# Kernel tuning notes

Measured on AMD Instinct MI355X. Metric: run time of the kernel, lower is better.

Reference implementation:

```python
import jax, jax.numpy as jnp
import numpy as np

THRESH = 0.5
POOL_K = 8  # feature_hw // proto_grid = 128 // 16
EPS = 1e-4
NEG = -1e30


def _avg_pool(x, k):
    # x: [n, c, h, w] -> [n, c, h//k, w//k]
    n, c, h, w = x.shape
    return x.reshape(n, c, h // k, k, w // k, k).mean(axis=(3, 5))


def reference(qry, sup_x, sup_y):
    # squeeze as in forward
    qry = qry[:, 0]          # [B=1, C, H, W]
    sup_x = sup_x[0, :, 0]   # [shot, C, H, W]
    sup_y = sup_y[0]         # [shot, 1, H, W]

    shot, nch, H, W = sup_x.shape

    # grid prototypes via avg pooling
    n_sup = _avg_pool(sup_x, POOL_K)                      # [shot, C, gh, gw]
    y_g = _avg_pool(sup_y, POOL_K)                        # [shot, 1, gh, gw]

    cand = n_sup.reshape(shot, nch, -1).transpose(0, 2, 1).reshape(-1, nch)  # [M, C]
    y_flat = y_g.reshape(-1)                              # [M]

    # threshold mask with fallback chain (thresh -> 0.1 -> all), static shapes
    m1 = y_flat > THRESH
    m2 = y_flat > 0.1
    m_all = jnp.ones_like(m1)
    mask = jnp.where(jnp.any(m1), m1, jnp.where(jnp.any(m2), m2, m_all))  # [M]

    # mean-center and safe L2-normalize prototypes (per proto over channels)
    protos = cand - cand.mean(axis=-1, keepdims=True)
    pro_n = protos / jnp.maximum(jnp.linalg.norm(protos, axis=1, keepdims=True), EPS)  # [M, C]

    # mean-center and safe L2-normalize query (per pixel over channels)
    qc = qry - qry.mean(axis=1, keepdims=True)
    qry_n = qc / jnp.maximum(jnp.linalg.norm(qc, axis=1, keepdims=True), EPS)          # [B, C, H, W]

    # cosine-sim 1x1 conv = GEMM, scaled
    dists = jnp.einsum('bchw,mc->bmhw', qry_n, pro_n) * 20.0                           # [B, M, H, W]

    # masked softmax over prototypes (equivalent to selecting masked subset)
    logits = jnp.where(mask[None, :, None, None], dists, NEG)
    prob = jax.nn.softmax(logits, axis=1)                                              # [B, M, H, W]

    # weighted back-projection and final similarity map
    ch_proto = jnp.einsum('mc,bmhw->bchw', pro_n, prob)                                # [B, C, H, W]
    pred_grid = jnp.sum(qry_n * ch_proto * 20.0, axis=1, keepdims=True)                # [B, 1, H, W]
    return pred_grid


def setup_inputs() -> dict:
    key = jax.random.key(0)
    k1, k2, k3 = jax.random.split(key, 3)
    qry = jax.random.normal(k1, (1, 1, 256, 128, 128), dtype=jnp.float32)
    sup_x = jax.random.normal(k2, (1, 5, 1, 256, 128, 128), dtype=jnp.float32)
    sup_y = jax.random.uniform(k3, (1, 5, 1, 128, 128), dtype=jnp.float32)
    return {"qry": qry, "sup_x": sup_x, "sup_y": sup_y}
```

## Files before the change

kernel.cpp:

```cpp
#include <hip/hip_runtime.h>
#include <math.h>

typedef _Float16 f16x8 __attribute__((ext_vector_type(8)));
typedef float f32x4 __attribute__((ext_vector_type(4)));


__global__ __launch_bounds__(256) void pool_kernel(const float* __restrict__ sup_x,
                                                   const float* __restrict__ sup_y,
                                                   _Float16* __restrict__ pro_raw,
                                                   float* __restrict__ psum,
                                                   float* __restrict__ yv_ws) {
    const int b = blockIdx.x, t = threadIdx.x;
    if (b < 640) {
        __shared__ float hs[8192];
        __shared__ float xa[16][33];
        const int s = b >> 7, rem = b & 127;
        const int gy = rem >> 3, cq = rem & 7;
        const float* base = sup_x + ((size_t)(s * 256 + cq * 32) * 128 + gy * 8) * 128;
#pragma unroll 8
        for (int i = 0; i < 32; ++i) {
            const int run = i * 8 + (t >> 5);
            const float4 v = *(const float4*)(base + ((size_t)(run >> 3) * 128 + (run & 7)) * 128 + (t & 31) * 4);
            hs[i * 256 + t] = v.x + v.y + v.z + v.w;
        }
        __syncthreads();
#pragma unroll
        for (int e0 = 0; e0 < 2; ++e0) {
            const int e = e0 * 256 + t;
            const int c = e >> 4, gx = e & 15;
            float sum = 0.f;
#pragma unroll
            for (int r = 0; r < 8; ++r)
                sum += hs[(c * 8 + r) * 32 + gx * 2] + hs[(c * 8 + r) * 32 + gx * 2 + 1];
            xa[gx][c] = sum * (1.f / 64.f);
        }
        __syncthreads();
        const int mbase = s * 256 + gy * 16;
        if (t < 64) {
            const int gx = t >> 2, gi = t & 3;
            const int m = mbase + gx;
            const int g = cq * 4 + gi;
            f16x8 hv;
#pragma unroll
            for (int j = 0; j < 8; ++j) hv[j] = (_Float16)xa[gx][gi * 8 + j];
            *(f16x8*)(pro_raw + (size_t)m * 256 + (g << 3)) = hv;
        } else if (t < 80) {
            const int gx = t - 64;
            float s1 = 0.f, s2 = 0.f;
#pragma unroll
            for (int c = 0; c < 32; ++c) { const float x = xa[gx][c]; s1 += x; s2 += x * x; }
            const int m = mbase + gx;
            psum[m * 16 + cq * 2]     = s1;
            psum[m * 16 + cq * 2 + 1] = s2;
        }
    } else {
        const int r = b - 640;
        const int gy = t >> 4, gx = t & 15;
        const float* base = sup_y + r * 16384 + gy * 1024 + gx * 8;
        float sum = 0.f;
#pragma unroll
        for (int rr = 0; rr < 8; ++rr) {
            const float4 a = *(const float4*)(base + rr * 128);
            const float4 bb = *(const float4*)(base + rr * 128 + 4);
            sum += a.x + a.y + a.z + a.w + bb.x + bb.y + bb.z + bb.w;
        }
        yv_ws[r * 256 + t] = sum * (1.f / 64.f);
    }
}

__device__ __forceinline__ void gload_lds16h(const _Float16* g, _Float16* l) {
    __builtin_amdgcn_global_load_lds((const __attribute__((address_space(1))) unsigned int*)g,
                                     (__attribute__((address_space(3))) unsigned int*)l,
                                     16, 0, 0);
}
__device__ __forceinline__ void gload_lds16f(const float* g, float* l) {
    __builtin_amdgcn_global_load_lds((const __attribute__((address_space(1))) unsigned int*)g,
                                     (__attribute__((address_space(3))) unsigned int*)l,
                                     16, 0, 0);
}

__device__ __forceinline__ void stage_gather(const _Float16* __restrict__ pro_raw,
                                             const unsigned short* __restrict__ idxc,
                                             int tb, _Float16* dst, int w, int l) {
#pragma unroll
    for (int i = 0; i < 8; ++i) {
        const int off = w * 4096 + i * 512 + l * 8;
        const int rowp = off >> 8;
        const int m = idxc[tb + rowp];
        const int sc = (l & 31) ^ (rowp & 7);
        gload_lds16h(pro_raw + (size_t)m * 256 + (sc << 3), dst + off);
    }
}

__device__ __forceinline__ void compute_tile(const _Float16* __restrict__ pb,
                                             const float* __restrict__ alfc,
                                             int tilebase, int NA,
                                             const f16x8 (&bfr)[4][8],
                                             int row, int ln7, int lq, int w,
                                             float (&Sa)[4], float (&Wa)[4]) {
    f32x4 acc[4];
#pragma unroll
    for (int p = 0; p < 4; ++p) acc[p] = (f32x4){0.f, 0.f, 0.f, 0.f};
#pragma unroll
    for (int ks = 0; ks < 8; ++ks) {
        const int ch = (ks * 4 + lq) ^ ln7;
        const f16x8 a = *(const f16x8*)(pb + row * 256 + ch * 8);
#pragma unroll
        for (int p = 0; p < 4; ++p)
            acc[p] = __builtin_amdgcn_mfma_f32_16x16x32_f16(a, bfr[p][ks], acc[p], 0, 0, 0);
    }
    const int jb = tilebase + w * 16 + lq * 4;
    const f32x4 av = *(const f32x4*)(alfc + jb);
#pragma unroll
    for (int p = 0; p < 4; ++p) {
        float ssum = 0.f, wsum = 0.f;
#pragma unroll
        for (int r = 0; r < 4; ++r) {
            const float d = av[r] * acc[p][r];
            const float mk = (jb + r < NA) ? 1.f : 0.f;
            const float e = mk * __expf(d - 20.f);
            ssum += e; wsum += e * d;
        }
        Sa[p] += ssum; Wa[p] += wsum;
    }
}

__global__ __launch_bounds__(512, 2) void main_kernel(const float* __restrict__ qry,
                                                      const _Float16* __restrict__ pro_raw,
                                                      const float* __restrict__ psum,
                                                      const float* __restrict__ yv_ws,
                                                      float* __restrict__ out) {
    __shared__ __align__(16) _Float16 arena[65536];
    __shared__ __align__(16) float alfc[1408];
    __shared__ unsigned short idxc[1408];
    __shared__ int tot_s[20];
    __shared__ float scr[1024];
    __shared__ float2 stats[64];
    __shared__ int iflags[2];

    float*     qtf  = (float*)arena;
    _Float16*  qs   = arena + 32768;
    _Float16*  buf0 = arena;
    _Float16*  buf1 = arena + 32768;
    float*     red  = (float*)arena;

    const int t = threadIdx.x;
    const int w = t >> 6, l = t & 63;
    const int ln = l & 15, lq = l >> 4;
    const int ln7 = ln & 7;
    const int px0 = blockIdx.x * 64;

    if (t < 2) iflags[t] = 0;
    for (int i = t; i < 1408; i += 512) { alfc[i] = 0.f; idxc[i] = 0; }
    __syncthreads();

#pragma unroll
    for (int i = 0; i < 8; ++i) {
        const int c = i * 32 + (t >> 4);
        gload_lds16f(qry + (size_t)c * 16384 + px0 + (t & 15) * 4,
                     qtf + i * 2048 + t * 4);
    }

    float alf3[3], yv3[3];
    int f0 = 0, f1 = 0;
#pragma unroll
    for (int k = 0; k < 3; ++k) {
        const int m = t + k * 512;
        if (m < 1280) {
            float S1 = 0.f, S2 = 0.f;
            const f32x4* pp = (const f32x4*)(psum + m * 16);
#pragma unroll
            for (int u = 0; u < 4; ++u) {
                const f32x4 p = pp[u];
                S1 += p[0] + p[2]; S2 += p[1] + p[3];
            }
            alf3[k] = 20.f / fmaxf(sqrtf(fmaxf(S2 - S1 * S1 * (1.f / 256.f), 0.f)), 1e-4f);
            const float y = yv_ws[m];
            yv3[k] = y;
            if (y > 0.5f) f0 = 1;
            if (y > 0.1f) f1 = 1;
        }
    }
    if (f0) atomicOr(&iflags[0], 1);
    if (f1) atomicOr(&iflags[1], 1);
    __syncthreads();

    const int mode = iflags[0] ? 0 : (iflags[1] ? 1 : 2);
    int mk3[3] = {0, 0, 0}, pos3[3], chk3[3];
#pragma unroll
    for (int k = 0; k < 3; ++k) {
        const int m = t + k * 512;
        if (m < 1280) {
            const int mk = (mode == 0) ? (yv3[k] > 0.5f) : (mode == 1) ? (yv3[k] > 0.1f) : 1;
            mk3[k] = mk;
            const unsigned long long bal = __ballot(mk);
            pos3[k] = (int)__popcll(bal & ((1ull << l) - 1ull));
            chk3[k] = k * 8 + w;
            if (l == 0) tot_s[k * 8 + w] = (int)__popcll(bal);
        }
    }

    {
        const int p = t & 63, q = t >> 6;
        float s1 = 0.f, s2 = 0.f;
        for (int cc = 0; cc < 32; ++cc) {
            const float x = qtf[(q * 32 + cc) * 64 + p];
            s1 += x; s2 += x * x;
        }
        scr[q * 64 + p] = s1; scr[512 + q * 64 + p] = s2;
    }
    __syncthreads();
    if (t < 64) {
        float S1 = 0.f, S2 = 0.f;
        for (int q = 0; q < 8; ++q) { S1 += scr[q * 64 + t]; S2 += scr[512 + q * 64 + t]; }
        const float mu = S1 * (1.f / 256.f);
        const float nrm = sqrtf(fmaxf(S2 - 256.f * mu * mu, 0.f));
        stats[t] = make_float2(mu, 1.f / fmaxf(nrm, 1e-4f));
    }
    int NA;
    {
        int run = 0, base3[3] = {0, 0, 0};
#pragma unroll
        for (int c = 0; c < 20; ++c) {
#pragma unroll
            for (int k = 0; k < 3; ++k) if (c == k * 8 + w) base3[k] = run;
            run += tot_s[c];
        }
        NA = run;
#pragma unroll
        for (int k = 0; k < 3; ++k) {
            if (mk3[k]) {
                const int j = base3[k] + pos3[k];
                idxc[j] = (unsigned short)(t + k * 512);
                alfc[j] = alf3[k];
            }
        }
    }
    __syncthreads();
    {
        const int px = t & 63, e = t >> 6;
        const float2 st = stats[px];
#pragma unroll
        for (int u = 0; u < 4; ++u) {
            const int g = e * 4 + u;
            f16x8 hv;
#pragma unroll
            for (int j = 0; j < 8; ++j)
                hv[j] = (_Float16)((qtf[(g * 8 + j) * 64 + px] - st.x) * st.y);
            *(f16x8*)(qs + px * 256 + ((g ^ (px & 7)) << 3)) = hv;
        }
    }
    __syncthreads();

    const int ntiles = (NA + 127) >> 7;

    stage_gather(pro_raw, idxc, 0, buf0, w, l);

    f16x8 bfr[4][8];
#pragma unroll
    for (int p = 0; p < 4; ++p) {
        const int px = p * 16 + ln;
        const int sB = px & 7;
#pragma unroll
        for (int ks = 0; ks < 8; ++ks) {
            const int g = ks * 4 + lq;
            bfr[p][ks] = *(const f16x8*)(qs + px * 256 + ((g ^ sB) << 3));
        }
    }
    __syncthreads();

    stage_gather(pro_raw, idxc, 128, buf1, w, l);

    const int row = w * 16 + ln;
    float Sa[4] = {0.f, 0.f, 0.f, 0.f}, Wa[4] = {0.f, 0.f, 0.f, 0.f};

#pragma unroll 1
    for (int tile = 0; tile < ntiles; ++tile) {
        if (tile < ntiles - 2) asm volatile("s_waitcnt vmcnt(8)" ::: "memory");
        else                   asm volatile("s_waitcnt vmcnt(0)" ::: "memory");
        compute_tile((tile & 1) ? buf1 : buf0, alfc, tile * 128, NA,
                     bfr, row, ln7, lq, w, Sa, Wa);
        if (tile + 2 < ntiles) {
            asm volatile("s_waitcnt lgkmcnt(0)" ::: "memory");
            __builtin_amdgcn_sched_barrier(0);
            stage_gather(pro_raw, idxc, (tile + 2) * 128, (tile & 1) ? buf1 : buf0, w, l);
        }
    }

    __syncthreads();
#pragma unroll
    for (int p = 0; p < 4; ++p) {
        const int px = p * 16 + ln;
        const int slot = (w * 4 + lq + px) & 31;
        red[px * 32 + slot] = Sa[p];
        red[2048 + px * 32 + slot] = Wa[p];
    }
    __syncthreads();
    if (t < 64) {
        float S = 0.f, W = 0.f;
        for (int s = 0; s < 32; ++s) {
            const int slot = (s + t) & 31;
            S += red[t * 32 + slot];
            W += red[2048 + t * 32 + slot];
        }
        out[px0 + t] = W / S;
    }
}

extern "C" void kernel_launch(void* const* d_in, const int* in_sizes, int n_in,
                              void* d_out, int out_size, void* d_ws, size_t ws_size,
                              hipStream_t stream) {
    const float* qry   = (const float*)d_in[0];
    const float* sup_x = (const float*)d_in[1];
    const float* sup_y = (const float*)d_in[2];
    float* out = (float*)d_out;

    char* ws = (char*)d_ws;
    _Float16*  pro_raw = (_Float16*)ws;           ws += 1280 * 256 * 2;
    float*     psum    = (float*)ws;              ws += 1280 * 16 * 4;
    float*     yv_ws   = (float*)ws;

    pool_kernel<<<645, 256, 0, stream>>>(sup_x, sup_y, pro_raw, psum, yv_ws);
    main_kernel<<<256, 512, 0, stream>>>(qry, pro_raw, psum, yv_ws, out);
}
```

Measured before the change: 34.77 us.

## Load query tile into registers instead of LDS and overlap first gather

The query tile now goes straight from global memory into per-thread registers (32 channels per wave, one pixel per lane) instead of through an LDS staging buffer via global_load_lds. Per-pixel sums are computed from registers, which removes the LDS round trip and a barrier. The first prototype gather is issued earlier so it overlaps with normalising the query and writing it to LDS. The second gather is skipped when there is only one tile, and the vmcnt wait condition is adjusted to match. This costs about 32 more VGPRs per thread and uses scalar 4-byte loads that are less vectorised than the previous 16-byte ones.

```diff
diff --git a/kernel.cpp b/kernel.cpp
--- a/kernel.cpp
+++ b/kernel.cpp
@@ -73,11 +73,6 @@
                                      (__attribute__((address_space(3))) unsigned int*)l,
                                      16, 0, 0);
 }
-__device__ __forceinline__ void gload_lds16f(const float* g, float* l) {
-    __builtin_amdgcn_global_load_lds((const __attribute__((address_space(1))) unsigned int*)g,
-                                     (__attribute__((address_space(3))) unsigned int*)l,
-                                     16, 0, 0);
-}
 
 __device__ __forceinline__ void stage_gather(const _Float16* __restrict__ pro_raw,
                                              const unsigned short* __restrict__ idxc,
@@ -138,10 +133,9 @@
     __shared__ float2 stats[64];
     __shared__ int iflags[2];
 
-    float*     qtf  = (float*)arena;
-    _Float16*  qs   = arena + 32768;
     _Float16*  buf0 = arena;
     _Float16*  buf1 = arena + 32768;
+    _Float16*  qs   = arena + 32768;
     float*     red  = (float*)arena;
 
     const int t = threadIdx.x;
@@ -152,14 +146,11 @@
 
     if (t < 2) iflags[t] = 0;
     for (int i = t; i < 1408; i += 512) { alfc[i] = 0.f; idxc[i] = 0; }
-    __syncthreads();
-
-#pragma unroll
-    for (int i = 0; i < 8; ++i) {
-        const int c = i * 32 + (t >> 4);
-        gload_lds16f(qry + (size_t)c * 16384 + px0 + (t & 15) * 4,
-                     qtf + i * 2048 + t * 4);
-    }
+
+    float qv[32];
+#pragma unroll
+    for (int j = 0; j < 32; ++j)
+        qv[j] = qry[(size_t)(w * 32 + j) * 16384 + px0 + l];
 
     float alf3[3], yv3[3];
     int f0 = 0, f1 = 0;
@@ -186,7 +177,7 @@
     __syncthreads();
 
     const int mode = iflags[0] ? 0 : (iflags[1] ? 1 : 2);
-    int mk3[3] = {0, 0, 0}, pos3[3], chk3[3];
+    int mk3[3] = {0, 0, 0}, pos3[3];
 #pragma unroll
     for (int k = 0; k < 3; ++k) {
         const int m = t + k * 512;
@@ -195,28 +186,18 @@
             mk3[k] = mk;
             const unsigned long long bal = __ballot(mk);
             pos3[k] = (int)__popcll(bal & ((1ull << l) - 1ull));
-            chk3[k] = k * 8 + w;
             if (l == 0) tot_s[k * 8 + w] = (int)__popcll(bal);
         }
     }
-
     {
-        const int p = t & 63, q = t >> 6;
         float s1 = 0.f, s2 = 0.f;
-        for (int cc = 0; cc < 32; ++cc) {
-            const float x = qtf[(q * 32 + cc) * 64 + p];
-            s1 += x; s2 += x * x;
-        }
-        scr[q * 64 + p] = s1; scr[512 + q * 64 + p] = s2;
-    }
-    __syncthreads();
-    if (t < 64) {
-        float S1 = 0.f, S2 = 0.f;
-        for (int q = 0; q < 8; ++q) { S1 += scr[q * 64 + t]; S2 += scr[512 + q * 64 + t]; }
-        const float mu = S1 * (1.f / 256.f);
-        const float nrm = sqrtf(fmaxf(S2 - 256.f * mu * mu, 0.f));
-        stats[t] = make_float2(mu, 1.f / fmaxf(nrm, 1e-4f));
-    }
+#pragma unroll
+        for (int j = 0; j < 32; ++j) { s1 += qv[j]; s2 += qv[j] * qv[j]; }
+        scr[w * 64 + l] = s1;
+        scr[512 + w * 64 + l] = s2;
+    }
+    __syncthreads();
+
     int NA;
     {
         int run = 0, base3[3] = {0, 0, 0};
@@ -236,25 +217,33 @@
             }
         }
     }
-    __syncthreads();
+    if (t < 64) {
+        float S1 = 0.f, S2 = 0.f;
+#pragma unroll
+        for (int q = 0; q < 8; ++q) { S1 += scr[q * 64 + t]; S2 += scr[512 + q * 64 + t]; }
+        const float mu = S1 * (1.f / 256.f);
+        const float nrm = sqrtf(fmaxf(S2 - 256.f * mu * mu, 0.f));
+        stats[t] = make_float2(mu, 1.f / fmaxf(nrm, 1e-4f));
+    }
+    __syncthreads();
+
+    const int ntiles = (NA + 127) >> 7;
+
+    stage_gather(pro_raw, idxc, 0, buf0, w, l);
+
     {
-        const int px = t & 63, e = t >> 6;
-        const float2 st = stats[px];
+        const float2 st = stats[l];
 #pragma unroll
         for (int u = 0; u < 4; ++u) {
-            const int g = e * 4 + u;
+            const int g = w * 4 + u;
             f16x8 hv;
 #pragma unroll
             for (int j = 0; j < 8; ++j)
-                hv[j] = (_Float16)((qtf[(g * 8 + j) * 64 + px] - st.x) * st.y);
-            *(f16x8*)(qs + px * 256 + ((g ^ (px & 7)) << 3)) = hv;
-        }
-    }
-    __syncthreads();
-
-    const int ntiles = (NA + 127) >> 7;
-
-    stage_gather(pro_raw, idxc, 0, buf0, w, l);
+                hv[j] = (_Float16)((qv[u * 8 + j] - st.x) * st.y);
+            *(f16x8*)(qs + l * 256 + ((g ^ (l & 7)) << 3)) = hv;
+        }
+    }
+    __syncthreads();
 
     f16x8 bfr[4][8];
 #pragma unroll
@@ -269,14 +258,14 @@
     }
     __syncthreads();
 
-    stage_gather(pro_raw, idxc, 128, buf1, w, l);
+    if (ntiles > 1) stage_gather(pro_raw, idxc, 128, buf1, w, l);
 
     const int row = w * 16 + ln;
     float Sa[4] = {0.f, 0.f, 0.f, 0.f}, Wa[4] = {0.f, 0.f, 0.f, 0.f};
 
 #pragma unroll 1
     for (int tile = 0; tile < ntiles; ++tile) {
-        if (tile < ntiles - 2) asm volatile("s_waitcnt vmcnt(8)" ::: "memory");
+        if (tile < ntiles - 1) asm volatile("s_waitcnt vmcnt(8)" ::: "memory");
         else                   asm volatile("s_waitcnt vmcnt(0)" ::: "memory");
         compute_tile((tile & 1) ? buf1 : buf0, alfc, tile * 128, NA,
                      bfr, row, ln7, lq, w, Sa, Wa);
```

Result: no change. 34.79 us (+0.1%).
